# Optimization experiments

Measured on AMD Instinct MI355X. Metric: run time of the kernel, lower is better.

## Reference

```python
import jax, jax.numpy as jnp
import numpy as np

N_QUBITS = 10
DIM = 2 ** N_QUBITS
W_MUL = (2 ** 0.5) * 5 ** (-0.5)  # he_std * lrmul with gain=sqrt(2), use_wscale=True, lrmul=1
C64 = jnp.complex64


def _rx(t):
    c = jnp.cos(t / 2).astype(C64)
    s = (-1j * jnp.sin(t / 2)).astype(C64)
    return jnp.stack([jnp.stack([c, s]), jnp.stack([s, c])])


def _ry(t):
    c = jnp.cos(t / 2).astype(C64)
    s = jnp.sin(t / 2).astype(C64)
    return jnp.stack([jnp.stack([c, -s]), jnp.stack([s, c])])


def _rz(t):
    e0 = jnp.exp(-1j * t.astype(C64) / 2)
    e1 = jnp.exp(1j * t.astype(C64) / 2)
    z = jnp.zeros((), C64)
    return jnp.stack([jnp.stack([e0, z]), jnp.stack([z, e1])])


def _apply_1q(U, g, q, n):
    # left-multiply full gate (I x g x I) @ U without materializing the kron
    U = U.reshape(2 ** q, 2, -1)  # (pre, qubit, rest*cols)
    U = jnp.einsum('ab,xby->xay', g, U)
    return U.reshape(2 ** n, 2 ** n)


def _apply_cnot(U, c, t, n):
    # left-multiply CNOT(control=c, target=t) @ U; qubit 0 is most significant
    dim = 2 ** n
    T = U.reshape((2,) * n + (-1,))
    flipped = jnp.flip(T, axis=t)  # X on target
    res = jnp.stack([jnp.take(T, 0, axis=c), jnp.take(flipped, 1, axis=c)], axis=c)
    return res.reshape(dim, dim)


def _circuit_unitary(w, n):
    U = jnp.eye(2 ** n, dtype=C64)
    for q in range(n):
        U = _apply_1q(U, _rx(w[6 * q + 0]), q, n)
        U = _apply_1q(U, _ry(w[6 * q + 1]), q, n)
        U = _apply_1q(U, _rz(w[6 * q + 2]), q, n)
    for q in range(n - 1):
        U = _apply_cnot(U, q, q + 1, n)
    U = _apply_cnot(U, n - 1, 0, n)
    for q in range(n):
        U = _apply_1q(U, _rx(w[6 * q + 3]), q, n)
        U = _apply_1q(U, _ry(w[6 * q + 4]), q, n)
        U = _apply_1q(U, _rz(w[6 * q + 5]), q, n)
    return U


def _ptrace(rho, dA, dB):
    # trace out the second subsystem: (dA,dB,dA,dB) -> (dA,dA)
    return jnp.einsum('ibjb->ij', rho.reshape(dA, dB, dA, dB))


def setup_inputs() -> dict:
    key = jax.random.key(0)
    k1, k2, k3 = jax.random.split(key, 3)
    inputA = jax.random.normal(k1, (32, 32), dtype=jnp.float32)
    inputB = jax.random.normal(k2, (32, 32), dtype=jnp.float32)
    weight = jax.random.uniform(k3, (6 * N_QUBITS,), minval=0.0,
                                maxval=2 * np.pi, dtype=jnp.float32)
    return {"inputA": inputA, "inputB": inputB, "weight": weight,
            "dimA": 32, "dimB": 32}


def reference(inputA, inputB, weight, dimA, dimB):
    w = weight * W_MUL
    U = _circuit_unitary(w, N_QUBITS)
    Ud = U.conj().T
    A = inputA.astype(C64)
    B = inputB.astype(C64)
    rhoAB = jnp.kron(A, B)
    U_AB = U @ rhoAB @ Ud
    rhoBA = jnp.kron(B, A)
    U_BA = U @ rhoBA @ Ud
    mutualBatA = _ptrace(U_AB, dimA, dimB)
    mutualAatB = _ptrace(U_BA, dimB, dimA)
    return (mutualBatA, mutualAatB)
```

## Files before the change

### kernel.cpp

```cpp
#include <hip/hip_runtime.h>

#define WMUL 0.63245553203367586640f

struct cplx { float re, im; };
struct __align__(16) cplx2 { cplx a, b; };

__device__ __forceinline__ cplx cmul(cplx a, cplx b) {
    return { a.re*b.re - a.im*b.im, a.re*b.im + a.im*b.re };
}
__device__ __forceinline__ cplx cmacc(cplx acc, cplx a, cplx b) {
    acc.re += a.re*b.re - a.im*b.im;
    acc.im += a.re*b.im + a.im*b.re;
    return acc;
}

__global__ __launch_bounds__(256)
void qmutual_kernel(const float* __restrict__ A, const float* __restrict__ B,
                    const float* __restrict__ weight, float* __restrict__ out,
                    int out_size)
{
    __shared__ __align__(16) cplx arena[7360];
    cplx* CLA   = arena;
    cplx* CLB   = arena + 1024;
    cplx* CL2A  = arena + 2048;
    cplx* TAT   = arena + 3072;
    cplx* TBT   = arena + 4160;
    cplx* A1p   = arena + 5248;
    cplx* B1p   = arena + 6304;
    cplx* Np    = arena;
    cplx* TFT   = arena + 3072;
    cplx* gates = arena + 5248;

    const int tid = threadIdx.x;
    const int i0 = tid >> 4, j0 = tid & 15;
    const int r0 = 2*i0, c0 = 2*j0;
    const int blk = blockIdx.x;
    const float* MA = blk ? B : A;
    const float* MB = blk ? A : B;

    if (tid < 20) {
        const int layer = tid / 10, q = tid % 10;
        const float w0 = weight[6*q + 3*layer + 0] * WMUL;
        const float w1 = weight[6*q + 3*layer + 1] * WMUL;
        const float w2 = weight[6*q + 3*layer + 2] * WMUL;
        const float cx = cosf(0.5f*w0), sx = sinf(0.5f*w0);
        const float cy = cosf(0.5f*w1), sy = sinf(0.5f*w1);
        const float cz = cosf(0.5f*w2), sz = sinf(0.5f*w2);
        cplx rx[2][2] = { { {cx,0.f}, {0.f,-sx} }, { {0.f,-sx}, {cx,0.f} } };
        cplx ry[2][2] = { { {cy,0.f}, {-sy,0.f} }, { {sy,0.f}, {cy,0.f} } };
        const cplx rz0 = {cz, -sz}, rz1 = {cz, sz};
        cplx m[2][2];
        #pragma unroll
        for (int r = 0; r < 2; ++r)
            #pragma unroll
            for (int c = 0; c < 2; ++c)
                m[r][c] = cmacc(cmul(ry[r][0], rx[0][c]), ry[r][1], rx[1][c]);
        cplx* g = gates + tid*4;
        g[0] = cmul(rz0, m[0][0]); g[1] = cmul(rz0, m[0][1]);
        g[2] = cmul(rz1, m[1][0]); g[3] = cmul(rz1, m[1][1]);
    }
    __syncthreads();

    {
        cplx vals[3][2][2];
        #pragma unroll
        for (int mat = 0; mat < 3; ++mat) {
            const int gbase = (mat == 0) ? 0 : (mat == 1 ? 5 : 10);
            #pragma unroll
            for (int kk = 0; kk < 2; ++kk)
                #pragma unroll
                for (int jj = 0; jj < 2; ++jj) {
                    const int k = r0 + kk, j = c0 + jj;
                    cplx v = {1.f, 0.f};
                    #pragma unroll
                    for (int q = 0; q < 5; ++q) {
                        const int rb = (j >> (4-q)) & 1;
                        const int cb = (k >> (4-q)) & 1;
                        v = cmul(v, gates[(gbase+q)*4 + rb*2 + cb]);
                    }
                    vals[mat][kk][jj] = { v.re, -v.im };
                }
        }
        #pragma unroll
        for (int kk = 0; kk < 2; ++kk) {
            *(cplx2*)&CLA [(r0+kk)*32 + c0] = { vals[0][kk][0], vals[0][kk][1] };
            *(cplx2*)&CLB [(r0+kk)*32 + c0] = { vals[1][kk][0], vals[1][kk][1] };
            *(cplx2*)&CL2A[(r0+kk)*32 + c0] = { vals[2][kk][0], vals[2][kk][1] };
        }
    }
    __syncthreads();

    {
        cplx ta[2][2] = {}, tb[2][2] = {};
        #pragma unroll
        for (int k = 0; k < 32; ++k) {
            const cplx2 xa = *(const cplx2*)&CLA[k*32 + r0];
            const cplx2 xb = *(const cplx2*)&CLB[k*32 + r0];
            const float2 ma = *(const float2*)&MA[k*32 + c0];
            const float2 mb = *(const float2*)&MB[k*32 + c0];
            ta[0][0].re += xa.a.re*ma.x; ta[0][0].im -= xa.a.im*ma.x;
            ta[0][1].re += xa.a.re*ma.y; ta[0][1].im -= xa.a.im*ma.y;
            ta[1][0].re += xa.b.re*ma.x; ta[1][0].im -= xa.b.im*ma.x;
            ta[1][1].re += xa.b.re*ma.y; ta[1][1].im -= xa.b.im*ma.y;
            tb[0][0].re += xb.a.re*mb.x; tb[0][0].im -= xb.a.im*mb.x;
            tb[0][1].re += xb.a.re*mb.y; tb[0][1].im -= xb.a.im*mb.y;
            tb[1][0].re += xb.b.re*mb.x; tb[1][0].im -= xb.b.im*mb.x;
            tb[1][1].re += xb.b.re*mb.y; tb[1][1].im -= xb.b.im*mb.y;
        }
        #pragma unroll
        for (int g = 0; g < 2; ++g) {
            *(cplx2*)&TAT[(c0+g)*34 + r0] = { ta[0][g], ta[1][g] };
            *(cplx2*)&TBT[(c0+g)*34 + r0] = { tb[0][g], tb[1][g] };
        }
    }
    __syncthreads();

    {
        cplx a1[2][2] = {}, b1[2][2] = {};
        #pragma unroll
        for (int k = 0; k < 32; ++k) {
            const cplx2 t  = *(const cplx2*)&TAT[k*34 + r0];
            const cplx2 u  = *(const cplx2*)&TBT[k*34 + r0];
            const cplx2 ca = *(const cplx2*)&CLA[k*32 + c0];
            const cplx2 cb = *(const cplx2*)&CLB[k*32 + c0];
            a1[0][0] = cmacc(a1[0][0], t.a, ca.a); a1[0][1] = cmacc(a1[0][1], t.a, ca.b);
            a1[1][0] = cmacc(a1[1][0], t.b, ca.a); a1[1][1] = cmacc(a1[1][1], t.b, ca.b);
            b1[0][0] = cmacc(b1[0][0], u.a, cb.a); b1[0][1] = cmacc(b1[0][1], u.a, cb.b);
            b1[1][0] = cmacc(b1[1][0], u.b, cb.a); b1[1][1] = cmacc(b1[1][1], u.b, cb.b);
        }
        #pragma unroll
        for (int p = 0; p < 2; ++p)
            #pragma unroll
            for (int g = 0; g < 2; ++g) {
                A1p[(r0+p)*33 + c0+g] = a1[p][g];
                B1p[(r0+p)*33 + c0+g] = b1[p][g];
            }
    }
    __syncthreads();

    {
        const int gr0 = r0 ^ (r0 >> 1), gr1 = (r0+1) ^ ((r0+1) >> 1);
        const int gc0 = c0 ^ (c0 >> 1), gc1 = (c0+1) ^ ((c0+1) >> 1);
        cplx n[2][2] = {};
        #pragma unroll
        for (int kb = 0; kb < 32; ++kb) {
            const int t24 = (kb & 1) ? 24 : 0;
            const int g   = kb ^ (kb >> 1);
            const int ar0 = gr0 ^ t24, ar1 = gr1 ^ t24;
            const int ac0 = gc0 ^ t24, ac1 = gc1 ^ t24;
            const cplx A00 = A1p[ar0*33 + ac0], A01 = A1p[ar0*33 + ac1];
            const cplx A10 = A1p[ar1*33 + ac0], A11 = A1p[ar1*33 + ac1];
            const cplx B00 = B1p[g*33 + g],          B01 = B1p[g*33 + (16^g)];
            const cplx B10 = B1p[(16^g)*33 + g],     B11 = B1p[(16^g)*33 + (16^g)];
            n[0][0] = cmacc(n[0][0], A00, B00); n[0][1] = cmacc(n[0][1], A01, B01);
            n[1][0] = cmacc(n[1][0], A10, B10); n[1][1] = cmacc(n[1][1], A11, B11);
        }
        __syncthreads();
        #pragma unroll
        for (int p = 0; p < 2; ++p)
            *(cplx2*)&Np[(r0+p)*34 + c0] = { n[p][0], n[p][1] };
    }
    __syncthreads();

    {
        cplx tf[2][2] = {};
        #pragma unroll
        for (int k = 0; k < 32; ++k) {
            const cplx2 x = *(const cplx2*)&CL2A[k*32 + r0];
            const cplx2 m = *(const cplx2*)&Np[k*34 + c0];
            tf[0][0].re += x.a.re*m.a.re + x.a.im*m.a.im;
            tf[0][0].im += x.a.re*m.a.im - x.a.im*m.a.re;
            tf[0][1].re += x.a.re*m.b.re + x.a.im*m.b.im;
            tf[0][1].im += x.a.re*m.b.im - x.a.im*m.b.re;
            tf[1][0].re += x.b.re*m.a.re + x.b.im*m.a.im;
            tf[1][0].im += x.b.re*m.a.im - x.b.im*m.a.re;
            tf[1][1].re += x.b.re*m.b.re + x.b.im*m.b.im;
            tf[1][1].im += x.b.re*m.b.im - x.b.im*m.b.re;
        }
        __syncthreads();
        #pragma unroll
        for (int g = 0; g < 2; ++g)
            *(cplx2*)&TFT[(c0+g)*34 + r0] = { tf[0][g], tf[1][g] };
    }
    __syncthreads();

    {
        cplx rr[2][2] = {};
        #pragma unroll
        for (int k = 0; k < 32; ++k) {
            const cplx2 t  = *(const cplx2*)&TFT[k*34 + r0];
            const cplx2 c2 = *(const cplx2*)&CL2A[k*32 + c0];
            rr[0][0] = cmacc(rr[0][0], t.a, c2.a); rr[0][1] = cmacc(rr[0][1], t.a, c2.b);
            rr[1][0] = cmacc(rr[1][0], t.b, c2.a); rr[1][1] = cmacc(rr[1][1], t.b, c2.b);
        }
        if (out_size >= 4096) {
            #pragma unroll
            for (int p = 0; p < 2; ++p) {
                float4 v = { rr[p][0].re, rr[p][0].im, rr[p][1].re, rr[p][1].im };
                *(float4*)&out[blk*2048 + (r0+p)*64 + 4*j0] = v;
            }
        } else {
            #pragma unroll
            for (int p = 0; p < 2; ++p) {
                float2 v = { rr[p][0].re, rr[p][1].re };
                *(float2*)&out[blk*1024 + (r0+p)*32 + c0] = v;
            }
        }
    }
}

extern "C" void kernel_launch(void* const* d_in, const int* in_sizes, int n_in,
                              void* d_out, int out_size, void* d_ws, size_t ws_size,
                              hipStream_t stream) {
    const float* A = (const float*)d_in[0];
    const float* B = (const float*)d_in[1];
    const float* w = (const float*)d_in[2];
    float* out = (float*)d_out;
    qmutual_kernel<<<2, 256, 0, stream>>>(A, B, w, out, out_size);
}
```

Baseline: 74.86 us.

## Use packed FP32 complex FMAs and precompute B-side partial-trace sums

Replaces the scalar complex multiply-accumulates in all matrix-product stages with inline-asm v_pk_fma_f32 pairs that use op_sel and negation modifiers. Separately, the 32-step N-stage loop is restructured algebraically: eight threads presum the B1 diagonal-block entries by parity into a small array, and every thread then does only two complex FMAs per output. This cuts FP instruction count and LDS reads in a latency-bound single-workgroup kernel. In exchange it adds one barrier, relies on hand-written asm modifiers being correct, and reorders float summation.

```diff
diff --git a/kernel.cpp b/kernel.cpp
--- a/kernel.cpp
+++ b/kernel.cpp
@@ -2,16 +2,36 @@
 
 #define WMUL 0.63245553203367586640f
 
-struct cplx { float re, im; };
-struct __align__(16) cplx2 { cplx a, b; };
-
-__device__ __forceinline__ cplx cmul(cplx a, cplx b) {
-    return { a.re*b.re - a.im*b.im, a.re*b.im + a.im*b.re };
-}
-__device__ __forceinline__ cplx cmacc(cplx acc, cplx a, cplx b) {
-    acc.re += a.re*b.re - a.im*b.im;
-    acc.im += a.re*b.im + a.im*b.re;
+typedef float v2f __attribute__((ext_vector_type(2)));
+typedef float v4f __attribute__((ext_vector_type(4)));
+
+__device__ __forceinline__ v4f cat(v2f a, v2f b) { return __builtin_shufflevector(a, b, 0, 1, 2, 3); }
+__device__ __forceinline__ v2f lo2(v4f t) { return __builtin_shufflevector(t, t, 0, 1); }
+__device__ __forceinline__ v2f hi2(v4f t) { return __builtin_shufflevector(t, t, 2, 3); }
+
+__device__ __forceinline__ v2f cmul_c(v2f a, v2f b) {
+    v2f r = { a.x*b.x - a.y*b.y, a.x*b.y + a.y*b.x };
+    return r;
+}
+__device__ __forceinline__ v2f cmacc_c(v2f acc, v2f a, v2f b) {
+    acc.x += a.x*b.x - a.y*b.y;
+    acc.y += a.x*b.y + a.y*b.x;
     return acc;
+}
+
+__device__ __forceinline__ void cmacc_pk(v2f& d, v2f a, v2f b) {
+    asm("v_pk_fma_f32 %0, %1, %2, %0 op_sel_hi:[0,1,1]\n\t"
+        "v_pk_fma_f32 %0, %1, %2, %0 op_sel:[1,1,0] op_sel_hi:[1,0,1] neg_lo:[1,0,0]"
+        : "+v"(d) : "v"(a), "v"(b));
+}
+__device__ __forceinline__ void cmacc_cj_pk(v2f& d, v2f a, v2f b) {
+    asm("v_pk_fma_f32 %0, %1, %2, %0 op_sel_hi:[0,1,1]\n\t"
+        "v_pk_fma_f32 %0, %1, %2, %0 op_sel:[1,1,0] op_sel_hi:[1,0,1] neg_hi:[1,0,0]"
+        : "+v"(d) : "v"(a), "v"(b));
+}
+__device__ __forceinline__ void cmacc_rj_pk(v2f& d, v2f a, v2f m) {
+    asm("v_pk_fma_f32 %0, %1, %2, %0 neg_hi:[1,0,0]"
+        : "+v"(d) : "v"(a), "v"(m));
 }
 
 __global__ __launch_bounds__(256)
@@ -19,17 +39,18 @@
                     const float* __restrict__ weight, float* __restrict__ out,
                     int out_size)
 {
-    __shared__ __align__(16) cplx arena[7360];
-    cplx* CLA   = arena;
-    cplx* CLB   = arena + 1024;
-    cplx* CL2A  = arena + 2048;
-    cplx* TAT   = arena + 3072;
-    cplx* TBT   = arena + 4160;
-    cplx* A1p   = arena + 5248;
-    cplx* B1p   = arena + 6304;
-    cplx* Np    = arena;
-    cplx* TFT   = arena + 3072;
-    cplx* gates = arena + 5248;
+    __shared__ __align__(16) v2f arena[7360];
+    v2f* CLA   = arena;
+    v2f* CLB   = arena + 1024;
+    v2f* CL2A  = arena + 2048;
+    v2f* TAT   = arena + 3072;
+    v2f* TBT   = arena + 4160;
+    v2f* A1p   = arena + 5248;
+    v2f* B1p   = arena + 6304;
+    v2f* Sarr  = arena + 3072;
+    v2f* Np    = arena;
+    v2f* TFT   = arena + 3072;
+    v2f* gates = arena + 5248;
 
     const int tid = threadIdx.x;
     const int i0 = tid >> 4, j0 = tid & 15;
@@ -46,23 +67,23 @@
         const float cx = cosf(0.5f*w0), sx = sinf(0.5f*w0);
         const float cy = cosf(0.5f*w1), sy = sinf(0.5f*w1);
         const float cz = cosf(0.5f*w2), sz = sinf(0.5f*w2);
-        cplx rx[2][2] = { { {cx,0.f}, {0.f,-sx} }, { {0.f,-sx}, {cx,0.f} } };
-        cplx ry[2][2] = { { {cy,0.f}, {-sy,0.f} }, { {sy,0.f}, {cy,0.f} } };
-        const cplx rz0 = {cz, -sz}, rz1 = {cz, sz};
-        cplx m[2][2];
+        v2f rx[2][2] = { { {cx,0.f}, {0.f,-sx} }, { {0.f,-sx}, {cx,0.f} } };
+        v2f ry[2][2] = { { {cy,0.f}, {-sy,0.f} }, { {sy,0.f}, {cy,0.f} } };
+        const v2f rz0 = {cz, -sz}, rz1 = {cz, sz};
+        v2f m[2][2];
         #pragma unroll
         for (int r = 0; r < 2; ++r)
             #pragma unroll
             for (int c = 0; c < 2; ++c)
-                m[r][c] = cmacc(cmul(ry[r][0], rx[0][c]), ry[r][1], rx[1][c]);
-        cplx* g = gates + tid*4;
-        g[0] = cmul(rz0, m[0][0]); g[1] = cmul(rz0, m[0][1]);
-        g[2] = cmul(rz1, m[1][0]); g[3] = cmul(rz1, m[1][1]);
-    }
-    __syncthreads();
-
-    {
-        cplx vals[3][2][2];
+                m[r][c] = cmacc_c(cmul_c(ry[r][0], rx[0][c]), ry[r][1], rx[1][c]);
+        v2f* g = gates + tid*4;
+        g[0] = cmul_c(rz0, m[0][0]); g[1] = cmul_c(rz0, m[0][1]);
+        g[2] = cmul_c(rz1, m[1][0]); g[3] = cmul_c(rz1, m[1][1]);
+    }
+    __syncthreads();
+
+    {
+        v2f vals[3][2][2];
         #pragma unroll
         for (int mat = 0; mat < 3; ++mat) {
             const int gbase = (mat == 0) ? 0 : (mat == 1 ? 5 : 10);
@@ -71,62 +92,65 @@
                 #pragma unroll
                 for (int jj = 0; jj < 2; ++jj) {
                     const int k = r0 + kk, j = c0 + jj;
-                    cplx v = {1.f, 0.f};
+                    v2f v = {1.f, 0.f};
                     #pragma unroll
                     for (int q = 0; q < 5; ++q) {
                         const int rb = (j >> (4-q)) & 1;
                         const int cb = (k >> (4-q)) & 1;
-                        v = cmul(v, gates[(gbase+q)*4 + rb*2 + cb]);
+                        v = cmul_c(v, gates[(gbase+q)*4 + rb*2 + cb]);
                     }
-                    vals[mat][kk][jj] = { v.re, -v.im };
+                    v2f cv = { v.x, -v.y };
+                    vals[mat][kk][jj] = cv;
                 }
         }
         #pragma unroll
         for (int kk = 0; kk < 2; ++kk) {
-            *(cplx2*)&CLA [(r0+kk)*32 + c0] = { vals[0][kk][0], vals[0][kk][1] };
-            *(cplx2*)&CLB [(r0+kk)*32 + c0] = { vals[1][kk][0], vals[1][kk][1] };
-            *(cplx2*)&CL2A[(r0+kk)*32 + c0] = { vals[2][kk][0], vals[2][kk][1] };
-        }
-    }
-    __syncthreads();
-
-    {
-        cplx ta[2][2] = {}, tb[2][2] = {};
-        #pragma unroll
-        for (int k = 0; k < 32; ++k) {
-            const cplx2 xa = *(const cplx2*)&CLA[k*32 + r0];
-            const cplx2 xb = *(const cplx2*)&CLB[k*32 + r0];
+            *(v4f*)&CLA [(r0+kk)*32 + c0] = cat(vals[0][kk][0], vals[0][kk][1]);
+            *(v4f*)&CLB [(r0+kk)*32 + c0] = cat(vals[1][kk][0], vals[1][kk][1]);
+            *(v4f*)&CL2A[(r0+kk)*32 + c0] = cat(vals[2][kk][0], vals[2][kk][1]);
+        }
+    }
+    __syncthreads();
+
+    {
+        v2f ta[2][2] = {}, tb[2][2] = {};
+        #pragma unroll
+        for (int k = 0; k < 32; ++k) {
+            const v4f xa = *(const v4f*)&CLA[k*32 + r0];
+            const v4f xb = *(const v4f*)&CLB[k*32 + r0];
             const float2 ma = *(const float2*)&MA[k*32 + c0];
             const float2 mb = *(const float2*)&MB[k*32 + c0];
-            ta[0][0].re += xa.a.re*ma.x; ta[0][0].im -= xa.a.im*ma.x;
-            ta[0][1].re += xa.a.re*ma.y; ta[0][1].im -= xa.a.im*ma.y;
-            ta[1][0].re += xa.b.re*ma.x; ta[1][0].im -= xa.b.im*ma.x;
-            ta[1][1].re += xa.b.re*ma.y; ta[1][1].im -= xa.b.im*ma.y;
-            tb[0][0].re += xb.a.re*mb.x; tb[0][0].im -= xb.a.im*mb.x;
-            tb[0][1].re += xb.a.re*mb.y; tb[0][1].im -= xb.a.im*mb.y;
-            tb[1][0].re += xb.b.re*mb.x; tb[1][0].im -= xb.b.im*mb.x;
-            tb[1][1].re += xb.b.re*mb.y; tb[1][1].im -= xb.b.im*mb.y;
+            const v2f xa0 = lo2(xa), xa1 = hi2(xa);
+            const v2f xb0 = lo2(xb), xb1 = hi2(xb);
+            const v2f mx = {ma.x, ma.x}, my = {ma.y, ma.y};
+            const v2f nx = {mb.x, mb.x}, ny = {mb.y, mb.y};
+            cmacc_rj_pk(ta[0][0], xa0, mx); cmacc_rj_pk(ta[0][1], xa0, my);
+            cmacc_rj_pk(ta[1][0], xa1, mx); cmacc_rj_pk(ta[1][1], xa1, my);
+            cmacc_rj_pk(tb[0][0], xb0, nx); cmacc_rj_pk(tb[0][1], xb0, ny);
+            cmacc_rj_pk(tb[1][0], xb1, nx); cmacc_rj_pk(tb[1][1], xb1, ny);
         }
         #pragma unroll
         for (int g = 0; g < 2; ++g) {
-            *(cplx2*)&TAT[(c0+g)*34 + r0] = { ta[0][g], ta[1][g] };
-            *(cplx2*)&TBT[(c0+g)*34 + r0] = { tb[0][g], tb[1][g] };
-        }
-    }
-    __syncthreads();
-
-    {
-        cplx a1[2][2] = {}, b1[2][2] = {};
-        #pragma unroll
-        for (int k = 0; k < 32; ++k) {
-            const cplx2 t  = *(const cplx2*)&TAT[k*34 + r0];
-            const cplx2 u  = *(const cplx2*)&TBT[k*34 + r0];
-            const cplx2 ca = *(const cplx2*)&CLA[k*32 + c0];
-            const cplx2 cb = *(const cplx2*)&CLB[k*32 + c0];
-            a1[0][0] = cmacc(a1[0][0], t.a, ca.a); a1[0][1] = cmacc(a1[0][1], t.a, ca.b);
-            a1[1][0] = cmacc(a1[1][0], t.b, ca.a); a1[1][1] = cmacc(a1[1][1], t.b, ca.b);
-            b1[0][0] = cmacc(b1[0][0], u.a, cb.a); b1[0][1] = cmacc(b1[0][1], u.a, cb.b);
-            b1[1][0] = cmacc(b1[1][0], u.b, cb.a); b1[1][1] = cmacc(b1[1][1], u.b, cb.b);
+            *(v4f*)&TAT[(c0+g)*34 + r0] = cat(ta[0][g], ta[1][g]);
+            *(v4f*)&TBT[(c0+g)*34 + r0] = cat(tb[0][g], tb[1][g]);
+        }
+    }
+    __syncthreads();
+
+    {
+        v2f a1[2][2] = {}, b1[2][2] = {};
+        #pragma unroll
+        for (int k = 0; k < 32; ++k) {
+            const v4f t  = *(const v4f*)&TAT[k*34 + r0];
+            const v4f u  = *(const v4f*)&TBT[k*34 + r0];
+            const v4f ca = *(const v4f*)&CLA[k*32 + c0];
+            const v4f cb = *(const v4f*)&CLB[k*32 + c0];
+            const v2f t0 = lo2(t), t1 = hi2(t), u0 = lo2(u), u1 = hi2(u);
+            const v2f ca0 = lo2(ca), ca1 = hi2(ca), cb0 = lo2(cb), cb1 = hi2(cb);
+            cmacc_pk(a1[0][0], t0, ca0); cmacc_pk(a1[0][1], t0, ca1);
+            cmacc_pk(a1[1][0], t1, ca0); cmacc_pk(a1[1][1], t1, ca1);
+            cmacc_pk(b1[0][0], u0, cb0); cmacc_pk(b1[0][1], u0, cb1);
+            cmacc_pk(b1[1][0], u1, cb0); cmacc_pk(b1[1][1], u1, cb1);
         }
         #pragma unroll
         for (int p = 0; p < 2; ++p)
@@ -138,71 +162,71 @@
     }
     __syncthreads();
 
+    if (tid < 8) {
+        const int p = (tid >> 2) & 1, eps = (tid >> 1) & 1, del = tid & 1;
+        v2f s = {0.f, 0.f};
+        #pragma unroll
+        for (int m = 0; m < 16; ++m) {
+            const int kb = 2*m + p;
+            const int g  = kb ^ (kb >> 1);
+            s += B1p[((eps<<4)^g)*33 + ((del<<4)^g)];
+        }
+        Sarr[tid] = s;
+    }
+    __syncthreads();
+
     {
         const int gr0 = r0 ^ (r0 >> 1), gr1 = (r0+1) ^ ((r0+1) >> 1);
         const int gc0 = c0 ^ (c0 >> 1), gc1 = (c0+1) ^ ((c0+1) >> 1);
-        cplx n[2][2] = {};
-        #pragma unroll
-        for (int kb = 0; kb < 32; ++kb) {
-            const int t24 = (kb & 1) ? 24 : 0;
-            const int g   = kb ^ (kb >> 1);
-            const int ar0 = gr0 ^ t24, ar1 = gr1 ^ t24;
-            const int ac0 = gc0 ^ t24, ac1 = gc1 ^ t24;
-            const cplx A00 = A1p[ar0*33 + ac0], A01 = A1p[ar0*33 + ac1];
-            const cplx A10 = A1p[ar1*33 + ac0], A11 = A1p[ar1*33 + ac1];
-            const cplx B00 = B1p[g*33 + g],          B01 = B1p[g*33 + (16^g)];
-            const cplx B10 = B1p[(16^g)*33 + g],     B11 = B1p[(16^g)*33 + (16^g)];
-            n[0][0] = cmacc(n[0][0], A00, B00); n[0][1] = cmacc(n[0][1], A01, B01);
-            n[1][0] = cmacc(n[1][0], A10, B10); n[1][1] = cmacc(n[1][1], A11, B11);
-        }
-        __syncthreads();
+        const v2f A00 = A1p[gr0*33 + gc0],        A01 = A1p[gr0*33 + gc1];
+        const v2f A10 = A1p[gr1*33 + gc0],        A11 = A1p[gr1*33 + gc1];
+        const v2f X00 = A1p[(gr0^24)*33 + (gc0^24)], X01 = A1p[(gr0^24)*33 + (gc1^24)];
+        const v2f X10 = A1p[(gr1^24)*33 + (gc0^24)], X11 = A1p[(gr1^24)*33 + (gc1^24)];
+        v2f n[2][2] = {};
+        cmacc_pk(n[0][0], A00, Sarr[0]); cmacc_pk(n[0][0], X00, Sarr[4]);
+        cmacc_pk(n[0][1], A01, Sarr[1]); cmacc_pk(n[0][1], X01, Sarr[5]);
+        cmacc_pk(n[1][0], A10, Sarr[2]); cmacc_pk(n[1][0], X10, Sarr[6]);
+        cmacc_pk(n[1][1], A11, Sarr[3]); cmacc_pk(n[1][1], X11, Sarr[7]);
         #pragma unroll
         for (int p = 0; p < 2; ++p)
-            *(cplx2*)&Np[(r0+p)*34 + c0] = { n[p][0], n[p][1] };
-    }
-    __syncthreads();
-
-    {
-        cplx tf[2][2] = {};
-        #pragma unroll
-        for (int k = 0; k < 32; ++k) {
-            const cplx2 x = *(const cplx2*)&CL2A[k*32 + r0];
-            const cplx2 m = *(const cplx2*)&Np[k*34 + c0];
-            tf[0][0].re += x.a.re*m.a.re + x.a.im*m.a.im;
-            tf[0][0].im += x.a.re*m.a.im - x.a.im*m.a.re;
-            tf[0][1].re += x.a.re*m.b.re + x.a.im*m.b.im;
-            tf[0][1].im += x.a.re*m.b.im - x.a.im*m.b.re;
-            tf[1][0].re += x.b.re*m.a.re + x.b.im*m.a.im;
-            tf[1][0].im += x.b.re*m.a.im - x.b.im*m.a.re;
-            tf[1][1].re += x.b.re*m.b.re + x.b.im*m.b.im;
-            tf[1][1].im += x.b.re*m.b.im - x.b.im*m.b.re;
-        }
-        __syncthreads();
+            *(v4f*)&Np[(r0+p)*34 + c0] = cat(n[p][0], n[p][1]);
+    }
+    __syncthreads();
+
+    {
+        v2f tf[2][2] = {};
+        #pragma unroll
+        for (int k = 0; k < 32; ++k) {
+            const v4f x = *(const v4f*)&CL2A[k*32 + r0];
+            const v4f m = *(const v4f*)&Np[k*34 + c0];
+            const v2f x0 = lo2(x), x1 = hi2(x), m0 = lo2(m), m1 = hi2(m);
+            cmacc_cj_pk(tf[0][0], x0, m0); cmacc_cj_pk(tf[0][1], x0, m1);
+            cmacc_cj_pk(tf[1][0], x1, m0); cmacc_cj_pk(tf[1][1], x1, m1);
+        }
         #pragma unroll
         for (int g = 0; g < 2; ++g)
-            *(cplx2*)&TFT[(c0+g)*34 + r0] = { tf[0][g], tf[1][g] };
-    }
-    __syncthreads();
-
-    {
-        cplx rr[2][2] = {};
-        #pragma unroll
-        for (int k = 0; k < 32; ++k) {
-            const cplx2 t  = *(const cplx2*)&TFT[k*34 + r0];
-            const cplx2 c2 = *(const cplx2*)&CL2A[k*32 + c0];
-            rr[0][0] = cmacc(rr[0][0], t.a, c2.a); rr[0][1] = cmacc(rr[0][1], t.a, c2.b);
-            rr[1][0] = cmacc(rr[1][0], t.b, c2.a); rr[1][1] = cmacc(rr[1][1], t.b, c2.b);
+            *(v4f*)&TFT[(c0+g)*34 + r0] = cat(tf[0][g], tf[1][g]);
+    }
+    __syncthreads();
+
+    {
+        v2f rr[2][2] = {};
+        #pragma unroll
+        for (int k = 0; k < 32; ++k) {
+            const v4f t  = *(const v4f*)&TFT[k*34 + r0];
+            const v4f c2 = *(const v4f*)&CL2A[k*32 + c0];
+            const v2f t0 = lo2(t), t1 = hi2(t), c20 = lo2(c2), c21 = hi2(c2);
+            cmacc_pk(rr[0][0], t0, c20); cmacc_pk(rr[0][1], t0, c21);
+            cmacc_pk(rr[1][0], t1, c20); cmacc_pk(rr[1][1], t1, c21);
         }
         if (out_size >= 4096) {
             #pragma unroll
+            for (int p = 0; p < 2; ++p)
+                *(v4f*)&out[blk*2048 + (r0+p)*64 + 4*j0] = cat(rr[p][0], rr[p][1]);
+        } else {
+            #pragma unroll
             for (int p = 0; p < 2; ++p) {
-                float4 v = { rr[p][0].re, rr[p][0].im, rr[p][1].re, rr[p][1].im };
-                *(float4*)&out[blk*2048 + (r0+p)*64 + 4*j0] = v;
-            }
-        } else {
-            #pragma unroll
-            for (int p = 0; p < 2; ++p) {
-                float2 v = { rr[p][0].re, rr[p][1].re };
+                float2 v = { rr[p][0].x, rr[p][1].x };
                 *(float2*)&out[blk*1024 + (r0+p)*32 + c0] = v;
             }
         }
```

After: 66.75 us. -10.8%, faster.
